# Kernel optimization log

Hardware: AMD Instinct MI355X
Metric: run time of the kernel (lower is better)

Reference implementation:

```python
import jax, jax.numpy as jnp
import numpy as np

EPS = 1e-5


def _create_scalars(x0, x, N, basis, v):
    # x0: [b,NT,3], x/v: [b,NT,ND,3], N: [b,NT], basis: [b,Nb,3]
    b, NT, ND, _ = x.shape
    v0 = jnp.mean(v, axis=2)                       # [b,NT,3]
    v = v - v0[:, :, None, :]
    feats = []
    # local_N normalization (log scaling)
    Nn = jnp.log1p(N.astype(x.dtype))
    feats.append(jnp.broadcast_to(Nn[:, :, None, None], (b, NT, ND, 1)))
    x0n = jnp.linalg.norm(x0, axis=-1, keepdims=True) + EPS   # [b,NT,1]
    feats.append(jnp.broadcast_to(x0n[:, :, None, :], (b, NT, ND, 1)))
    x0u = x0 / x0n
    x0b = jnp.einsum('bid,bjd->bij', x0u, basis)              # [b,NT,Nb]
    feats.append(jnp.broadcast_to(x0b[:, :, None, :], (b, NT, ND, x0b.shape[-1])))
    v0n = jnp.linalg.norm(v0, axis=-1, keepdims=True) + EPS
    feats.append(jnp.broadcast_to(v0n[:, :, None, :], (b, NT, ND, 1)))
    v0u = v0 / v0n
    v0b = jnp.einsum('bid,bjd->bij', v0u, basis)
    feats.append(jnp.broadcast_to(v0b[:, :, None, :], (b, NT, ND, v0b.shape[-1])))
    x0v0 = jnp.einsum('bid,bid->bi', x0u, v0u)                # [b,NT]
    feats.append(jnp.broadcast_to(x0v0[:, :, None, None], (b, NT, ND, 1)))
    xn = jnp.linalg.norm(x, axis=-1, keepdims=True) + EPS     # [b,NT,ND,1]
    feats.append(xn)
    xu = x / xn
    feats.append(jnp.einsum('bijd,bkd->bijk', xu, basis))     # [b,NT,ND,Nb]
    vn = jnp.linalg.norm(v, axis=-1, keepdims=True) + EPS
    feats.append(vn)
    vu = v / vn
    feats.append(jnp.einsum('bijd,bkd->bijk', vu, basis))
    feats.append(jnp.einsum('bijd,bijd->bij', xu, vu)[..., None])
    return jnp.concatenate(feats, axis=-1)                    # [b,NT,ND,19]


def setup_inputs() -> dict:
    key = jax.random.key(0)
    ks = jax.random.split(key, 12)
    b, NT, ND, Nb = 4, 1024, 128, 3
    k_in, H, L = 19, 256, 128
    s0 = 1.0 / np.sqrt(k_in)
    s1 = 1.0 / np.sqrt(H)
    return {
        'x0': jax.random.normal(ks[0], (b, NT, 3), jnp.float32),
        'x': jax.random.normal(ks[1], (b, NT, ND, 3), jnp.float32),
        'N': jax.random.randint(ks[2], (b, NT), 1, 1000),
        'basis': jax.random.normal(ks[3], (b, Nb, 3), jnp.float32),
        'v': jax.random.normal(ks[4], (b, NT, ND, 3), jnp.float32),
        'W0': jax.random.normal(ks[5], (k_in, H), jnp.float32) * s0,
        'b0': jnp.zeros((H,), jnp.float32),
        'W1': jax.random.normal(ks[6], (H, H), jnp.float32) * s1,
        'b1': jnp.zeros((H,), jnp.float32),
        'W2': jax.random.normal(ks[7], (H, L), jnp.float32) * s1,
        'b2': jnp.zeros((L,), jnp.float32),
    }


def reference(x0, x, N, basis, v, W0, b0, W1, b1, W2, b2):
    s = _create_scalars(x0, x, N, basis, v)            # [b,NT,ND,19]
    h = jax.nn.leaky_relu(s @ W0 + b0)                 # layer 0 MLP
    h = jnp.mean(h, axis=2)                            # pool over N_DM -> [b,NT,H]
    h = jax.nn.leaky_relu(h @ W1 + b1)                 # layer 1
    return h @ W2 + b2                                 # layer 2 -> [b,NT,Nlatent]
```

## Files before the change

### kernel.cpp

```cpp
#include <hip/hip_runtime.h>
#include <math.h>

#define EPSF 1e-5f
constexpr int NT  = 1024;
constexpr int ND  = 128;
constexpr int KIN = 19;
constexpr int H   = 256;
constexpr int L   = 128;
constexpr int T   = 4;

typedef __attribute__((ext_vector_type(8))) short short8;
typedef __attribute__((ext_vector_type(4))) float f32x4;

static __device__ inline unsigned cvt_pk_bf16(float lo, float hi) {
    unsigned r;
    asm("v_cvt_pk_bf16_f32 %0, %1, %2" : "=v"(r) : "v"(lo), "v"(hi));
    return r;
}

__global__ __launch_bounds__(256) void k_feat_l0(
    const float* __restrict__ x0, const float* __restrict__ x,
    const int*   __restrict__ Nv, const float* __restrict__ basis,
    const float* __restrict__ v,  const float* __restrict__ W0,
    const float* __restrict__ b0, float* __restrict__ hm_out)
{
    const int tid  = threadIdx.x;
    const int lane = tid & 63;
    const int w    = tid >> 6;
    const int g    = blockIdx.x * T + w;
    const int bidx = g >> 10;

    __shared__ __align__(16) ushort featb[T * 512 * 8];

    short8 bfrag[4];
    {
        const int col16 = lane & 15;
        const int kb    = lane >> 4;
        #pragma unroll
        for (int nt = 0; nt < 4; ++nt) {
            const int col = w * 64 + nt * 16 + col16;
            float fv[8];
            #pragma unroll
            for (int j = 0; j < 8; ++j) {
                const int k = kb * 8 + j;
                fv[j] = (k < KIN) ? W0[k * H + col] : ((k == KIN) ? b0[col] : 0.f);
            }
            uint4 pk;
            pk.x = cvt_pk_bf16(fv[0], fv[1]);
            pk.y = cvt_pk_bf16(fv[2], fv[3]);
            pk.z = cvt_pk_bf16(fv[4], fv[5]);
            pk.w = cvt_pk_bf16(fv[6], fv[7]);
            bfrag[nt] = *reinterpret_cast<short8*>(&pk);
        }
    }

    const float* xp = x + (size_t)g * (ND * 3);
    const float* vp = v + (size_t)g * (ND * 3);
    float X[2][3], V[2][3];
    #pragma unroll
    for (int i = 0; i < 2; ++i) {
        const int d = lane + i * 64;
        X[i][0] = xp[d*3+0]; X[i][1] = xp[d*3+1]; X[i][2] = xp[d*3+2];
        V[i][0] = vp[d*3+0]; V[i][1] = vp[d*3+1]; V[i][2] = vp[d*3+2];
    }

    float sx = V[0][0] + V[1][0];
    float sy = V[0][1] + V[1][1];
    float sz = V[0][2] + V[1][2];
    #pragma unroll
    for (int m = 1; m < 64; m <<= 1) {
        sx += __shfl_xor(sx, m, 64);
        sy += __shfl_xor(sy, m, 64);
        sz += __shfl_xor(sz, m, 64);
    }
    const float invd = 1.0f / (float)ND;
    const float v0x = sx * invd, v0y = sy * invd, v0z = sz * invd;

    float fs[10];
    {
        const float ax = x0[g*3+0], ay = x0[g*3+1], az = x0[g*3+2];
        const float x0n = sqrtf(ax*ax + ay*ay + az*az) + EPSF;
        const float v0n = sqrtf(v0x*v0x + v0y*v0y + v0z*v0z) + EPSF;
        const float ix  = 1.f / x0n, iv0 = 1.f / v0n;
        const float* bs = basis + bidx * 9;
        fs[0] = log1pf((float)Nv[g]);
        fs[1] = x0n;
        fs[2] = (ax*bs[0] + ay*bs[1] + az*bs[2]) * ix;
        fs[3] = (ax*bs[3] + ay*bs[4] + az*bs[5]) * ix;
        fs[4] = (ax*bs[6] + ay*bs[7] + az*bs[8]) * ix;
        fs[5] = v0n;
        fs[6] = (v0x*bs[0] + v0y*bs[1] + v0z*bs[2]) * iv0;
        fs[7] = (v0x*bs[3] + v0y*bs[4] + v0z*bs[5]) * iv0;
        fs[8] = (v0x*bs[6] + v0y*bs[7] + v0z*bs[8]) * iv0;
        fs[9] = (ax*v0x + ay*v0y + az*v0z) * ix * iv0;
    }

    const float* bs = basis + bidx * 9;
    #pragma unroll
    for (int i = 0; i < 2; ++i) {
        const int d  = lane + i * 64;
        const float cx = V[i][0] - v0x, cy = V[i][1] - v0y, cz = V[i][2] - v0z;
        const float xx = X[i][0], xy = X[i][1], xz = X[i][2];
        const float xn = sqrtf(xx*xx + xy*xy + xz*xz) + EPSF;
        const float vn = sqrtf(cx*cx + cy*cy + cz*cz) + EPSF;
        const float ixn = 1.f/xn, ivn = 1.f/vn;
        float f[20];
        #pragma unroll
        for (int k = 0; k < 10; ++k) f[k] = fs[k];
        f[10] = xn;
        f[11] = (xx*bs[0] + xy*bs[1] + xz*bs[2]) * ixn;
        f[12] = (xx*bs[3] + xy*bs[4] + xz*bs[5]) * ixn;
        f[13] = (xx*bs[6] + xy*bs[7] + xz*bs[8]) * ixn;
        f[14] = vn;
        f[15] = (cx*bs[0] + cy*bs[1] + cz*bs[2]) * ivn;
        f[16] = (cx*bs[3] + cy*bs[4] + cz*bs[5]) * ivn;
        f[17] = (cx*bs[6] + cy*bs[7] + cz*bs[8]) * ivn;
        f[18] = (xx*cx + xy*cy + xz*cz) * ixn * ivn;
        f[19] = 1.0f;
        const int mt  = d >> 4;
        const int r16 = d & 15;
        uint4* base = reinterpret_cast<uint4*>(&featb[((w << 9) + (mt << 6) + r16) * 8]);
        uint4 pk0, pk1, pk2;
        pk0.x = cvt_pk_bf16(f[0],  f[1]);  pk0.y = cvt_pk_bf16(f[2],  f[3]);
        pk0.z = cvt_pk_bf16(f[4],  f[5]);  pk0.w = cvt_pk_bf16(f[6],  f[7]);
        pk1.x = cvt_pk_bf16(f[8],  f[9]);  pk1.y = cvt_pk_bf16(f[10], f[11]);
        pk1.z = cvt_pk_bf16(f[12], f[13]); pk1.w = cvt_pk_bf16(f[14], f[15]);
        pk2.x = cvt_pk_bf16(f[16], f[17]); pk2.y = cvt_pk_bf16(f[18], f[19]);
        pk2.z = 0u; pk2.w = 0u;
        base[0]  = pk0;
        base[16] = pk1;
        base[32] = pk2;
        base[48] = uint4{0u,0u,0u,0u};
    }
    __syncthreads();

    const f32x4 zc = {0.f, 0.f, 0.f, 0.f};
    #pragma unroll 1
    for (int t = 0; t < T; ++t) {
        f32x4 psum[4];
        #pragma unroll
        for (int nt = 0; nt < 4; ++nt)
            #pragma unroll
            for (int r = 0; r < 4; ++r) psum[nt][r] = 0.f;

        #pragma unroll
        for (int mt = 0; mt < 8; ++mt) {
            const short8 af = *reinterpret_cast<const short8*>(
                &featb[((t << 9) + (mt << 6) + lane) * 8]);
            #pragma unroll
            for (int nt = 0; nt < 4; ++nt) {
                f32x4 d = __builtin_amdgcn_mfma_f32_16x16x32_bf16(af, bfrag[nt], zc, 0, 0, 0);
                #pragma unroll
                for (int r = 0; r < 4; ++r) {
                    const float a = d[r];
                    psum[nt][r] = fmaf(0.505f, a, fmaf(0.495f, fabsf(a), psum[nt][r]));
                }
            }
        }

        const int gg = blockIdx.x * T + t;
        #pragma unroll
        for (int nt = 0; nt < 4; ++nt) {
            float s4 = psum[nt][0] + psum[nt][1] + psum[nt][2] + psum[nt][3];
            s4 += __shfl_xor(s4, 16, 64);
            s4 += __shfl_xor(s4, 32, 64);
            if (lane < 16)
                hm_out[(size_t)gg * H + w * 64 + nt * 16 + lane] = s4 * invd;
        }
    }
}

__global__ __launch_bounds__(256) void k_l12(
    const float* __restrict__ hm, const float* __restrict__ W1,
    const float* __restrict__ b1, const float* __restrict__ W2,
    const float* __restrict__ b2, float* __restrict__ out)
{
    const int tb  = blockIdx.x * 8;
    const int tid = threadIdx.x;
    __shared__ float hs[8][H];
    __shared__ float h1[8][H];

    {
        const float4* src = reinterpret_cast<const float4*>(hm + (size_t)tb * H);
        float4* dst = reinterpret_cast<float4*>(&hs[0][0]);
        #pragma unroll
        for (int i = 0; i < 2; ++i) dst[tid + i*256] = src[tid + i*256];
    }
    __syncthreads();

    {
        float acc[8];
        const float bb = b1[tid];
        #pragma unroll
        for (int t = 0; t < 8; ++t) acc[t] = bb;
        for (int k = 0; k < H; ++k) {
            const float w = W1[(size_t)k * H + tid];
            #pragma unroll
            for (int t = 0; t < 8; ++t) acc[t] = fmaf(hs[t][k], w, acc[t]);
        }
        #pragma unroll
        for (int t = 0; t < 8; ++t) {
            float a = acc[t];
            h1[t][tid] = (a > 0.f) ? a : 0.01f * a;
        }
    }
    __syncthreads();

    {
        const int n  = tid & 127;
        const int t0 = (tid >> 7) * 4;
        float acc[4];
        const float bb = b2[n];
        #pragma unroll
        for (int t = 0; t < 4; ++t) acc[t] = bb;
        for (int k = 0; k < H; ++k) {
            const float w = W2[(size_t)k * L + n];
            #pragma unroll
            for (int t = 0; t < 4; ++t) acc[t] = fmaf(h1[t0 + t][k], w, acc[t]);
        }
        #pragma unroll
        for (int t = 0; t < 4; ++t)
            out[(size_t)(tb + t0 + t) * L + n] = acc[t];
    }
}

extern "C" void kernel_launch(void* const* d_in, const int* in_sizes, int n_in,
                              void* d_out, int out_size, void* d_ws, size_t ws_size,
                              hipStream_t stream) {
    const float* x0    = (const float*)d_in[0];
    const float* x     = (const float*)d_in[1];
    const int*   Nv    = (const int*)  d_in[2];
    const float* basis = (const float*)d_in[3];
    const float* v     = (const float*)d_in[4];
    const float* W0    = (const float*)d_in[5];
    const float* b0    = (const float*)d_in[6];
    const float* W1    = (const float*)d_in[7];
    const float* b1    = (const float*)d_in[8];
    const float* W2    = (const float*)d_in[9];
    const float* b2    = (const float*)d_in[10];
    float* out = (float*)d_out;
    float* hm  = (float*)d_ws;

    hipLaunchKernelGGL(k_feat_l0, dim3(4 * NT / T), dim3(256), 0, stream,
                       x0, x, Nv, basis, v, W0, b0, hm);
    hipLaunchKernelGGL(k_l12, dim3(4 * NT / 8), dim3(256), 0, stream,
                       hm, W1, b1, W2, b2, out);
}
```

Baseline: 48.06 us.

## Process one particle group per block instead of four in feature/layer-0 kernel

Each block now handles one group (NT index) rather than four, giving four times more blocks. Two waves compute features for the 128 DM points, then all four waves do the MFMA layer-0 over the shared features for their own column slice. W0 fragment loading moves after the barrier, and shared memory shrinks to one group's tile. This gives more parallelism and lower LDS use per block, at the cost of reloading W0 fragments four times as often and leaving half the waves idle during feature computation.

```diff
diff --git a/kernel.cpp b/kernel.cpp
--- a/kernel.cpp
+++ b/kernel.cpp
@@ -7,7 +7,6 @@
 constexpr int KIN = 19;
 constexpr int H   = 256;
 constexpr int L   = 128;
-constexpr int T   = 4;
 
 typedef __attribute__((ext_vector_type(8))) short short8;
 typedef __attribute__((ext_vector_type(4))) float f32x4;
@@ -27,80 +26,58 @@
     const int tid  = threadIdx.x;
     const int lane = tid & 63;
     const int w    = tid >> 6;
-    const int g    = blockIdx.x * T + w;
+    const int g    = blockIdx.x;
     const int bidx = g >> 10;
 
-    __shared__ __align__(16) ushort featb[T * 512 * 8];
-
-    short8 bfrag[4];
-    {
-        const int col16 = lane & 15;
-        const int kb    = lane >> 4;
-        #pragma unroll
-        for (int nt = 0; nt < 4; ++nt) {
-            const int col = w * 64 + nt * 16 + col16;
-            float fv[8];
-            #pragma unroll
-            for (int j = 0; j < 8; ++j) {
-                const int k = kb * 8 + j;
-                fv[j] = (k < KIN) ? W0[k * H + col] : ((k == KIN) ? b0[col] : 0.f);
-            }
-            uint4 pk;
-            pk.x = cvt_pk_bf16(fv[0], fv[1]);
-            pk.y = cvt_pk_bf16(fv[2], fv[3]);
-            pk.z = cvt_pk_bf16(fv[4], fv[5]);
-            pk.w = cvt_pk_bf16(fv[6], fv[7]);
-            bfrag[nt] = *reinterpret_cast<short8*>(&pk);
-        }
-    }
-
-    const float* xp = x + (size_t)g * (ND * 3);
-    const float* vp = v + (size_t)g * (ND * 3);
-    float X[2][3], V[2][3];
-    #pragma unroll
-    for (int i = 0; i < 2; ++i) {
-        const int d = lane + i * 64;
-        X[i][0] = xp[d*3+0]; X[i][1] = xp[d*3+1]; X[i][2] = xp[d*3+2];
-        V[i][0] = vp[d*3+0]; V[i][1] = vp[d*3+1]; V[i][2] = vp[d*3+2];
-    }
-
-    float sx = V[0][0] + V[1][0];
-    float sy = V[0][1] + V[1][1];
-    float sz = V[0][2] + V[1][2];
-    #pragma unroll
-    for (int m = 1; m < 64; m <<= 1) {
-        sx += __shfl_xor(sx, m, 64);
-        sy += __shfl_xor(sy, m, 64);
-        sz += __shfl_xor(sz, m, 64);
-    }
-    const float invd = 1.0f / (float)ND;
-    const float v0x = sx * invd, v0y = sy * invd, v0z = sz * invd;
-
-    float fs[10];
-    {
-        const float ax = x0[g*3+0], ay = x0[g*3+1], az = x0[g*3+2];
-        const float x0n = sqrtf(ax*ax + ay*ay + az*az) + EPSF;
-        const float v0n = sqrtf(v0x*v0x + v0y*v0y + v0z*v0z) + EPSF;
-        const float ix  = 1.f / x0n, iv0 = 1.f / v0n;
+    __shared__ __align__(16) ushort featb[512 * 8];
+
+    if (w < 2) {
+        const float* xp = x + (size_t)g * (ND * 3);
+        const float* vp = v + (size_t)g * (ND * 3);
+        float V0[3], V1[3], X[3];
+        #pragma unroll
+        for (int j = 0; j < 3; ++j) {
+            V0[j] = vp[lane*3 + j];
+            V1[j] = vp[(lane + 64)*3 + j];
+            X[j]  = xp[(w*64 + lane)*3 + j];
+        }
+
+        float sx = V0[0] + V1[0];
+        float sy = V0[1] + V1[1];
+        float sz = V0[2] + V1[2];
+        #pragma unroll
+        for (int m = 1; m < 64; m <<= 1) {
+            sx += __shfl_xor(sx, m, 64);
+            sy += __shfl_xor(sy, m, 64);
+            sz += __shfl_xor(sz, m, 64);
+        }
+        const float invd = 1.0f / (float)ND;
+        const float v0x = sx * invd, v0y = sy * invd, v0z = sz * invd;
+
         const float* bs = basis + bidx * 9;
-        fs[0] = log1pf((float)Nv[g]);
-        fs[1] = x0n;
-        fs[2] = (ax*bs[0] + ay*bs[1] + az*bs[2]) * ix;
-        fs[3] = (ax*bs[3] + ay*bs[4] + az*bs[5]) * ix;
-        fs[4] = (ax*bs[6] + ay*bs[7] + az*bs[8]) * ix;
-        fs[5] = v0n;
-        fs[6] = (v0x*bs[0] + v0y*bs[1] + v0z*bs[2]) * iv0;
-        fs[7] = (v0x*bs[3] + v0y*bs[4] + v0z*bs[5]) * iv0;
-        fs[8] = (v0x*bs[6] + v0y*bs[7] + v0z*bs[8]) * iv0;
-        fs[9] = (ax*v0x + ay*v0y + az*v0z) * ix * iv0;
-    }
-
-    const float* bs = basis + bidx * 9;
-    #pragma unroll
-    for (int i = 0; i < 2; ++i) {
-        const int d  = lane + i * 64;
-        const float cx = V[i][0] - v0x, cy = V[i][1] - v0y, cz = V[i][2] - v0z;
-        const float xx = X[i][0], xy = X[i][1], xz = X[i][2];
+        float fs[10];
+        {
+            const float ax = x0[g*3+0], ay = x0[g*3+1], az = x0[g*3+2];
+            const float x0n = sqrtf(ax*ax + ay*ay + az*az) + EPSF;
+            const float v0n = sqrtf(v0x*v0x + v0y*v0y + v0z*v0z) + EPSF;
+            const float ix  = 1.f / x0n, iv0 = 1.f / v0n;
+            fs[0] = log1pf((float)Nv[g]);
+            fs[1] = x0n;
+            fs[2] = (ax*bs[0] + ay*bs[1] + az*bs[2]) * ix;
+            fs[3] = (ax*bs[3] + ay*bs[4] + az*bs[5]) * ix;
+            fs[4] = (ax*bs[6] + ay*bs[7] + az*bs[8]) * ix;
+            fs[5] = v0n;
+            fs[6] = (v0x*bs[0] + v0y*bs[1] + v0z*bs[2]) * iv0;
+            fs[7] = (v0x*bs[3] + v0y*bs[4] + v0z*bs[5]) * iv0;
+            fs[8] = (v0x*bs[6] + v0y*bs[7] + v0z*bs[8]) * iv0;
+            fs[9] = (ax*v0x + ay*v0y + az*v0z) * ix * iv0;
+        }
+
+        const float vx = (w == 0) ? V0[0] : V1[0];
+        const float vy = (w == 0) ? V0[1] : V1[1];
+        const float vz = (w == 0) ? V0[2] : V1[2];
+        const float cx = vx - v0x, cy = vy - v0y, cz = vz - v0z;
+        const float xx = X[0], xy = X[1], xz = X[2];
         const float xn = sqrtf(xx*xx + xy*xy + xz*xz) + EPSF;
         const float vn = sqrtf(cx*cx + cy*cy + cz*cz) + EPSF;
         const float ixn = 1.f/xn, ivn = 1.f/vn;
@@ -117,9 +94,10 @@
         f[17] = (cx*bs[6] + cy*bs[7] + cz*bs[8]) * ivn;
         f[18] = (xx*cx + xy*cy + xz*cz) * ixn * ivn;
         f[19] = 1.0f;
-        const int mt  = d >> 4;
-        const int r16 = d & 15;
-        uint4* base = reinterpret_cast<uint4*>(&featb[((w << 9) + (mt << 6) + r16) * 8]);
+
+        const int mt  = w * 4 + (lane >> 4);
+        const int r16 = lane & 15;
+        uint4* base = reinterpret_cast<uint4*>(&featb[((mt << 6) + r16) * 8]);
         uint4 pk0, pk1, pk2;
         pk0.x = cvt_pk_bf16(f[0],  f[1]);  pk0.y = cvt_pk_bf16(f[2],  f[3]);
         pk0.z = cvt_pk_bf16(f[4],  f[5]);  pk0.w = cvt_pk_bf16(f[6],  f[7]);
@@ -134,39 +112,58 @@
     }
     __syncthreads();
 
+    short8 bfrag[4];
+    {
+        const int col16 = lane & 15;
+        const int kb    = lane >> 4;
+        #pragma unroll
+        for (int nt = 0; nt < 4; ++nt) {
+            const int col = w * 64 + nt * 16 + col16;
+            float fv[8];
+            #pragma unroll
+            for (int j = 0; j < 8; ++j) {
+                const int k = kb * 8 + j;
+                fv[j] = (k < KIN) ? W0[k * H + col] : ((k == KIN) ? b0[col] : 0.f);
+            }
+            uint4 pk;
+            pk.x = cvt_pk_bf16(fv[0], fv[1]);
+            pk.y = cvt_pk_bf16(fv[2], fv[3]);
+            pk.z = cvt_pk_bf16(fv[4], fv[5]);
+            pk.w = cvt_pk_bf16(fv[6], fv[7]);
+            bfrag[nt] = *reinterpret_cast<short8*>(&pk);
+        }
+    }
+
     const f32x4 zc = {0.f, 0.f, 0.f, 0.f};
-    #pragma unroll 1
-    for (int t = 0; t < T; ++t) {
-        f32x4 psum[4];
-        #pragma unroll
-        for (int nt = 0; nt < 4; ++nt)
-            #pragma unroll
-            for (int r = 0; r < 4; ++r) psum[nt][r] = 0.f;
-
-        #pragma unroll
-        for (int mt = 0; mt < 8; ++mt) {
-            const short8 af = *reinterpret_cast<const short8*>(
-                &featb[((t << 9) + (mt << 6) + lane) * 8]);
-            #pragma unroll
-            for (int nt = 0; nt < 4; ++nt) {
-                f32x4 d = __builtin_amdgcn_mfma_f32_16x16x32_bf16(af, bfrag[nt], zc, 0, 0, 0);
-                #pragma unroll
-                for (int r = 0; r < 4; ++r) {
-                    const float a = d[r];
-                    psum[nt][r] = fmaf(0.505f, a, fmaf(0.495f, fabsf(a), psum[nt][r]));
-                }
+    f32x4 psum[4];
+    #pragma unroll
+    for (int nt = 0; nt < 4; ++nt)
+        #pragma unroll
+        for (int r = 0; r < 4; ++r) psum[nt][r] = 0.f;
+
+    #pragma unroll 2
+    for (int mt = 0; mt < 8; ++mt) {
+        const short8 af = *reinterpret_cast<const short8*>(
+            &featb[((mt << 6) + lane) * 8]);
+        #pragma unroll
+        for (int nt = 0; nt < 4; ++nt) {
+            f32x4 d = __builtin_amdgcn_mfma_f32_16x16x32_bf16(af, bfrag[nt], zc, 0, 0, 0);
+            #pragma unroll
+            for (int r = 0; r < 4; ++r) {
+                const float a = d[r];
+                psum[nt][r] = fmaf(0.505f, a, fmaf(0.495f, fabsf(a), psum[nt][r]));
             }
         }
-
-        const int gg = blockIdx.x * T + t;
-        #pragma unroll
-        for (int nt = 0; nt < 4; ++nt) {
-            float s4 = psum[nt][0] + psum[nt][1] + psum[nt][2] + psum[nt][3];
-            s4 += __shfl_xor(s4, 16, 64);
-            s4 += __shfl_xor(s4, 32, 64);
-            if (lane < 16)
-                hm_out[(size_t)gg * H + w * 64 + nt * 16 + lane] = s4 * invd;
-        }
+    }
+
+    const float invd = 1.0f / (float)ND;
+    #pragma unroll
+    for (int nt = 0; nt < 4; ++nt) {
+        float s4 = psum[nt][0] + psum[nt][1] + psum[nt][2] + psum[nt][3];
+        s4 += __shfl_xor(s4, 16, 64);
+        s4 += __shfl_xor(s4, 32, 64);
+        if (lane < 16)
+            hm_out[(size_t)g * H + w * 64 + nt * 16 + lane] = s4 * invd;
     }
 }
 
@@ -241,7 +238,7 @@
     float* out = (float*)d_out;
     float* hm  = (float*)d_ws;
 
-    hipLaunchKernelGGL(k_feat_l0, dim3(4 * NT / T), dim3(256), 0, stream,
+    hipLaunchKernelGGL(k_feat_l0, dim3(4 * NT), dim3(256), 0, stream,
                        x0, x, Nv, basis, v, W0, b0, hm);
     hipLaunchKernelGGL(k_l12, dim3(4 * NT / 8), dim3(256), 0, stream,
                        hm, W1, b1, W2, b2, out);
```

Measured after the change: 49.46 us. +2.9%, slower.
